# Kernel tuning notes

Measured on AMD Instinct MI355X. Metric: run time of the kernel, lower is better.

The kernel has to match this reference:

```python
import jax, jax.numpy as jnp
import numpy as np

EMBED_DIM = 128
NUM_HEADS = 4
HEAD_DIM = EMBED_DIM // NUM_HEADS


def setup_inputs() -> dict:
    key = jax.random.key(0)
    ks = jax.random.split(key, 9)
    B, C, H, W = 8, EMBED_DIM, 64, 64
    s = 1.0 / np.sqrt(EMBED_DIM)
    x = jax.random.normal(ks[0], (B, C, H, W), dtype=jnp.float32)
    Wq = jax.random.uniform(ks[1], (EMBED_DIM, EMBED_DIM), jnp.float32, -s, s)
    bq = jax.random.uniform(ks[2], (EMBED_DIM,), jnp.float32, -s, s)
    Wk = jax.random.uniform(ks[3], (EMBED_DIM, EMBED_DIM), jnp.float32, -s, s)
    bk = jax.random.uniform(ks[4], (EMBED_DIM,), jnp.float32, -s, s)
    Wv = jax.random.uniform(ks[5], (EMBED_DIM, EMBED_DIM), jnp.float32, -s, s)
    bv = jax.random.uniform(ks[6], (EMBED_DIM,), jnp.float32, -s, s)
    Wo = jax.random.uniform(ks[7], (EMBED_DIM, EMBED_DIM), jnp.float32, -s, s)
    bo = jax.random.uniform(ks[8], (EMBED_DIM,), jnp.float32, -s, s)
    return {"x": x, "Wq": Wq, "bq": bq, "Wk": Wk, "bk": bk,
            "Wv": Wv, "bv": bv, "Wo": Wo, "bo": bo}


def reference(x, Wq, bq, Wk, bk, Wv, bv, Wo, bo):
    B, C, H, W = x.shape
    N = H * W
    # (B, C, H, W) -> (B, N, C) tokens
    t = x.reshape(B, C, N).transpose(0, 2, 1)
    # torch Linear: y = t @ W.T + b
    Q = t @ Wq.T + bq
    K = t @ Wk.T + bk
    V = t @ Wv.T + bv
    # split heads: (B, heads, N, head_dim)
    Q = Q.reshape(B, N, NUM_HEADS, HEAD_DIM).transpose(0, 2, 1, 3)
    K = K.reshape(B, N, NUM_HEADS, HEAD_DIM).transpose(0, 2, 1, 3)
    V = V.reshape(B, N, NUM_HEADS, HEAD_DIM).transpose(0, 2, 1, 3)
    scale = 1.0 / np.sqrt(HEAD_DIM).astype(np.float32)
    attn = jnp.einsum('bhnd,bhmd->bhnm', Q, K) * scale  # (B,h,N,N)
    attn = jax.nn.softmax(attn, axis=-1)
    out = jnp.einsum('bhnm,bhmd->bhnd', attn, V)
    out = out.transpose(0, 2, 1, 3).reshape(B, N, EMBED_DIM)
    out = out @ Wo.T + bo
    return out.transpose(0, 2, 1).reshape(B, EMBED_DIM, H, W)
```

## Files before the change

kernel.cpp:

```cpp
#include <hip/hip_runtime.h>


using f32x4  = __attribute__((ext_vector_type(4))) float;
using bf16x8 = __attribute__((ext_vector_type(8))) short;

#define QSCALE 0.17677669529663687f
#define LOG2E  1.4426950408889634f
#define QKS    (QSCALE * LOG2E)

static __device__ __forceinline__ unsigned short f2bf(float f) {
    union { float f; unsigned int u; } v; v.f = f;
    unsigned int r = v.u + 0x7FFFu + ((v.u >> 16) & 1u);
    return (unsigned short)(r >> 16);
}

static __device__ __forceinline__ f32x4 mfma16(bf16x8 a, bf16x8 b, f32x4 c) {
    return __builtin_amdgcn_mfma_f32_16x16x32_bf16(a, b, c, 0, 0, 0);
}

__global__ __launch_bounds__(256) void k_prep(
    const float* __restrict__ x,
    const float* __restrict__ Wq, const float* __restrict__ Wk,
    const float* __restrict__ Wv, const float* __restrict__ Wo,
    unsigned short* __restrict__ t_bf, unsigned short* __restrict__ Wb)
{
    const int bx = blockIdx.x;
    const int tid = threadIdx.x;
    if (bx >= 1024) {
        const int m = bx - 1024;
        const float* W = (m == 0) ? Wq : (m == 1) ? Wk : (m == 2) ? Wv : Wo;
        const float s = (m == 0) ? QKS : 1.0f;
        for (int idx = tid; idx < 16384; idx += 256)
            Wb[m * 16384 + idx] = f2bf(W[idx] * s);
        return;
    }
    __shared__ float tl[64][65];
    const int b  = bx >> 7;
    const int c0 = ((bx >> 6) & 1) * 64;
    const int n0 = (bx & 63) * 64;
    for (int idx = tid; idx < 4096; idx += 256) {
        const int ci = idx >> 6, nj = idx & 63;
        tl[ci][nj] = x[((size_t)(b * 128 + c0 + ci)) * 4096 + n0 + nj];
    }
    __syncthreads();
    for (int idx = tid; idx < 4096; idx += 256) {
        const int nj = idx >> 6, ci = idx & 63;
        t_bf[((size_t)(b * 4096 + n0 + nj)) * 128 + c0 + ci] = f2bf(tl[ci][nj]);
    }
}

__global__ __launch_bounds__(256) void k_proj3(
    const unsigned short* __restrict__ t_bf, const unsigned short* __restrict__ Wb,
    const float* __restrict__ bq, const float* __restrict__ bk, const float* __restrict__ bv,
    unsigned short* __restrict__ Qb, unsigned short* __restrict__ Kb,
    unsigned short* __restrict__ Vt)
{
    const int mat  = blockIdx.y;
    const int widx = threadIdx.x >> 6;
    const int lane = threadIdx.x & 63;
    const int g = lane >> 4, l15 = lane & 15;
    const int row0 = blockIdx.x * 64 + widx * 16;
    const int gt_row = row0 + l15;
    const unsigned short* Wm = Wb + mat * 16384;
    const float* bias = (mat == 0) ? bq : (mat == 1) ? bk : bv;

    bf16x8 tf[4];
    #pragma unroll
    for (int kc = 0; kc < 4; ++kc)
        tf[kc] = *(const bf16x8*)(t_bf + (size_t)gt_row * 128 + kc * 32 + g * 8);

    #pragma unroll
    for (int ot = 0; ot < 8; ++ot) {
        f32x4 acc;
        if (mat < 2) {
            float bb = bias[ot * 16 + l15];
            if (mat == 0) bb *= QKS;
            acc[0] = bb; acc[1] = bb; acc[2] = bb; acc[3] = bb;
        } else {
            #pragma unroll
            for (int r = 0; r < 4; ++r) acc[r] = bias[ot * 16 + 4 * g + r];
        }
        #pragma unroll
        for (int kc = 0; kc < 4; ++kc) {
            bf16x8 wf = *(const bf16x8*)(Wm + (size_t)(ot * 16 + l15) * 128 + kc * 32 + g * 8);
            acc = (mat == 2) ? mfma16(wf, tf[kc], acc) : mfma16(tf[kc], wf, acc);
        }
        if (mat < 2) {
            unsigned short* dst = (mat == 0) ? Qb : Kb;
            const int o = ot * 16 + l15, h = o >> 5, d = o & 31;
            #pragma unroll
            for (int r = 0; r < 4; ++r) {
                const int gt = row0 + 4 * g + r;
                const int b = gt >> 12, n = gt & 4095;
                dst[(((size_t)(b * 4 + h)) * 4096 + n) * 32 + d] = f2bf(acc[r]);
            }
        } else {
            const int b = gt_row >> 12, n = gt_row & 4095;
            const int n31 = n & 31;
            const int pos = ((n31 >> 2) & 3) * 8 + ((n31 >> 4) & 1) * 4 + (n31 & 3);
            #pragma unroll
            for (int r = 0; r < 4; ++r) {
                const int o = ot * 16 + 4 * g + r, h2 = o >> 5, d = o & 31;
                const size_t tb2 = ((size_t)(b * 4 + h2) * 128 + ((n >> 5) & 127)) * 1024;
                Vt[tb2 + d * 32 + pos] = f2bf(acc[r]);
            }
        }
    }
}

__global__ __launch_bounds__(256) void k_attn(
    const unsigned short* __restrict__ Qb, const unsigned short* __restrict__ Kb,
    const unsigned short* __restrict__ Vt, unsigned short* __restrict__ Ob)
{
    const int bid = blockIdx.x;
    const int swz = (bid & 7) * 512 + (bid >> 3);
    const int widx = threadIdx.x >> 6;
    const int bh = swz >> 7, q0 = (swz & 127) * 32;
    const int lane = threadIdx.x & 63, g = lane >> 4, l15 = lane & 15;

    __shared__ float lacc[3][32][36];
    __shared__ float lden[3][32];

    const bf16x8 qf0 = *(const bf16x8*)(Qb + ((size_t)bh * 4096 + q0 + l15) * 32 + g * 8);
    const bf16x8 qf1 = *(const bf16x8*)(Qb + ((size_t)bh * 4096 + q0 + 16 + l15) * 32 + g * 8);

    const unsigned short* kp = Kb + (size_t)bh * 131072
                             + (size_t)(widx * 1024 + l15) * 32 + g * 8;
    const unsigned short* vp = Vt + (size_t)bh * 131072 + (size_t)widx * 32768
                             + l15 * 32 + g * 8;

    bf16x8 onesf;
    #pragma unroll
    for (int j = 0; j < 8; ++j) onesf[j] = (short)0x3F80;

    f32x4 acc00 = {0.f,0.f,0.f,0.f}, acc01 = {0.f,0.f,0.f,0.f};
    f32x4 acc10 = {0.f,0.f,0.f,0.f}, acc11 = {0.f,0.f,0.f,0.f};
    f32x4 acc20 = {0.f,0.f,0.f,0.f}, acc21 = {0.f,0.f,0.f,0.f};
    const f32x4 z = {0.f,0.f,0.f,0.f};

    #pragma unroll 2
    for (int it = 0; it < 32; ++it) {
        const bf16x8 kf0 = *(const bf16x8*)(kp);
        const bf16x8 kf1 = *(const bf16x8*)(kp + 512);
        const bf16x8 vf0 = *(const bf16x8*)(vp);
        const bf16x8 vf1 = *(const bf16x8*)(vp + 512);
        kp += 1024;
        vp += 1024;

        f32x4 s00 = mfma16(kf0, qf0, z), s01 = mfma16(kf1, qf0, z);
        f32x4 s10 = mfma16(kf0, qf1, z), s11 = mfma16(kf1, qf1, z);

        bf16x8 pa0, pa1;
        #pragma unroll
        for (int i = 0; i < 4; ++i) {
            pa0[i]     = (short)f2bf(__builtin_amdgcn_exp2f(s00[i]));
            pa0[4 + i] = (short)f2bf(__builtin_amdgcn_exp2f(s01[i]));
            pa1[i]     = (short)f2bf(__builtin_amdgcn_exp2f(s10[i]));
            pa1[4 + i] = (short)f2bf(__builtin_amdgcn_exp2f(s11[i]));
        }

        acc00 = mfma16(pa0, vf0, acc00);
        acc01 = mfma16(pa0, vf1, acc01);
        acc20 = mfma16(pa0, onesf, acc20);
        acc10 = mfma16(pa1, vf0, acc10);
        acc11 = mfma16(pa1, vf1, acc11);
        acc21 = mfma16(pa1, onesf, acc21);
    }

    if (widx != 0) {
        const int s = widx - 1;
        *(f32x4*)&lacc[s][l15][4 * g]           = acc00;
        *(f32x4*)&lacc[s][16 + l15][4 * g]      = acc01;
        *(f32x4*)&lacc[s][l15][16 + 4 * g]      = acc10;
        *(f32x4*)&lacc[s][16 + l15][16 + 4 * g] = acc11;
        if (l15 == 0) {
            #pragma unroll
            for (int r = 0; r < 4; ++r) {
                lden[s][4 * g + r]      = acc20[r];
                lden[s][16 + 4 * g + r] = acc21[r];
            }
        }
    }
    __syncthreads();
    if (widx != 0) return;

    const int b = bh >> 2, h = bh & 3;
    #pragma unroll
    for (int r = 0; r < 4; ++r) {
        const int row0 = 4 * g + r, row1 = 16 + 4 * g + r;
        const float rd0 = 1.0f / (acc20[r] + lden[0][row0] + lden[1][row0] + lden[2][row0]);
        const float rd1 = 1.0f / (acc21[r] + lden[0][row1] + lden[1][row1] + lden[2][row1]);
        const float o00 = acc00[r] + lacc[0][l15][row0]      + lacc[1][l15][row0]      + lacc[2][l15][row0];
        const float o01 = acc01[r] + lacc[0][16 + l15][row0] + lacc[1][16 + l15][row0] + lacc[2][16 + l15][row0];
        const float o10 = acc10[r] + lacc[0][l15][row1]      + lacc[1][l15][row1]      + lacc[2][l15][row1];
        const float o11 = acc11[r] + lacc[0][16 + l15][row1] + lacc[1][16 + l15][row1] + lacc[2][16 + l15][row1];
        const size_t base0 = ((size_t)b * 4096 + q0 + row0) * 128 + h * 32;
        const size_t base1 = ((size_t)b * 4096 + q0 + row1) * 128 + h * 32;
        Ob[base0 + l15]      = f2bf(o00 * rd0);
        Ob[base0 + 16 + l15] = f2bf(o01 * rd0);
        Ob[base1 + l15]      = f2bf(o10 * rd1);
        Ob[base1 + 16 + l15] = f2bf(o11 * rd1);
    }
}

__global__ __launch_bounds__(256) void k_projo(
    const unsigned short* __restrict__ Ob, const unsigned short* __restrict__ Wob,
    const float* __restrict__ bo, float* __restrict__ out)
{
    const int widx = threadIdx.x >> 6;
    const int lane = threadIdx.x & 63, g = lane >> 4, l15 = lane & 15;
    const int gt = blockIdx.x * 64 + widx * 16 + l15;
    const int b = gt >> 12, n = gt & 4095;

    bf16x8 of[4];
    #pragma unroll
    for (int kc = 0; kc < 4; ++kc)
        of[kc] = *(const bf16x8*)(Ob + (size_t)gt * 128 + kc * 32 + g * 8);

    #pragma unroll
    for (int ot = 0; ot < 8; ++ot) {
        f32x4 acc;
        #pragma unroll
        for (int r = 0; r < 4; ++r) acc[r] = bo[ot * 16 + 4 * g + r];
        #pragma unroll
        for (int kc = 0; kc < 4; ++kc) {
            bf16x8 wf = *(const bf16x8*)(Wob + (size_t)(ot * 16 + l15) * 128 + kc * 32 + g * 8);
            acc = mfma16(wf, of[kc], acc);
        }
        #pragma unroll
        for (int r = 0; r < 4; ++r)
            out[((size_t)b * 128 + ot * 16 + 4 * g + r) * 4096 + n] = acc[r];
    }
}

extern "C" void kernel_launch(void* const* d_in, const int* in_sizes, int n_in,
                              void* d_out, int out_size, void* d_ws, size_t ws_size,
                              hipStream_t stream)
{
    const float* x  = (const float*)d_in[0];
    const float* Wq = (const float*)d_in[1];
    const float* bq = (const float*)d_in[2];
    const float* Wk = (const float*)d_in[3];
    const float* bk = (const float*)d_in[4];
    const float* Wv = (const float*)d_in[5];
    const float* bv = (const float*)d_in[6];
    const float* Wo = (const float*)d_in[7];
    const float* bo = (const float*)d_in[8];
    float* out = (float*)d_out;

    char* ws = (char*)d_ws;
    unsigned short* t_bf = (unsigned short*)(ws);
    unsigned short* Wb   = (unsigned short*)(ws +  8388608);
    unsigned short* Qb   = (unsigned short*)(ws +  8519680);
    unsigned short* Kb   = (unsigned short*)(ws + 16908288);
    unsigned short* Vt   = (unsigned short*)(ws + 25296896);
    unsigned short* Ob   = (unsigned short*)(ws + 33685504);

    k_prep <<<dim3(1028),     dim3(256), 0, stream>>>(x, Wq, Wk, Wv, Wo, t_bf, Wb);
    k_proj3<<<dim3(512, 3),   dim3(256), 0, stream>>>(t_bf, Wb, bq, bk, bv, Qb, Kb, Vt);
    k_attn <<<dim3(4096),     dim3(256), 0, stream>>>(Qb, Kb, Vt, Ob);
    k_projo<<<dim3(512),      dim3(256), 0, stream>>>(Ob, Wb + 3 * 16384, bo, out);
}
```

Before: 184.7 us.

## Process 64 queries per attention block to reuse K/V loads across four fragments

The attention kernel now handles 64 query rows per block instead of 32, so each K/V fragment loaded from global memory feeds four query fragments rather than two, and the grid is halved. It also replaces the manual round-to-nearest bf16 conversion of the exponentiated scores with native __bf16 casts, which may lower to hardware conversion instructions. The trade-off is more accumulator registers and shared memory per block, which may reduce occupancy, and fewer blocks across the GPU.

```diff
diff --git a/kernel.cpp b/kernel.cpp
--- a/kernel.cpp
+++ b/kernel.cpp
@@ -3,6 +3,7 @@
 
 using f32x4  = __attribute__((ext_vector_type(4))) float;
 using bf16x8 = __attribute__((ext_vector_type(8))) short;
+using bfv8   = __attribute__((ext_vector_type(8))) __bf16;
 
 #define QSCALE 0.17677669529663687f
 #define LOG2E  1.4426950408889634f
@@ -113,16 +114,18 @@
     const unsigned short* __restrict__ Vt, unsigned short* __restrict__ Ob)
 {
     const int bid = blockIdx.x;
-    const int swz = (bid & 7) * 512 + (bid >> 3);
+    const int swz = (bid & 7) * 256 + (bid >> 3);
     const int widx = threadIdx.x >> 6;
-    const int bh = swz >> 7, q0 = (swz & 127) * 32;
+    const int bh = swz >> 6, q0 = (swz & 63) * 64;
     const int lane = threadIdx.x & 63, g = lane >> 4, l15 = lane & 15;
 
-    __shared__ float lacc[3][32][36];
-    __shared__ float lden[3][32];
-
-    const bf16x8 qf0 = *(const bf16x8*)(Qb + ((size_t)bh * 4096 + q0 + l15) * 32 + g * 8);
-    const bf16x8 qf1 = *(const bf16x8*)(Qb + ((size_t)bh * 4096 + q0 + 16 + l15) * 32 + g * 8);
+    __shared__ float lacc[3][32][68];
+    __shared__ float lden[3][64];
+
+    bf16x8 qf[4];
+    #pragma unroll
+    for (int f = 0; f < 4; ++f)
+        qf[f] = *(const bf16x8*)(Qb + ((size_t)bh * 4096 + q0 + f * 16 + l15) * 32 + g * 8);
 
     const unsigned short* kp = Kb + (size_t)bh * 131072
                              + (size_t)(widx * 1024 + l15) * 32 + g * 8;
@@ -133,12 +136,16 @@
     #pragma unroll
     for (int j = 0; j < 8; ++j) onesf[j] = (short)0x3F80;
 
-    f32x4 acc00 = {0.f,0.f,0.f,0.f}, acc01 = {0.f,0.f,0.f,0.f};
-    f32x4 acc10 = {0.f,0.f,0.f,0.f}, acc11 = {0.f,0.f,0.f,0.f};
-    f32x4 acc20 = {0.f,0.f,0.f,0.f}, acc21 = {0.f,0.f,0.f,0.f};
+    f32x4 aO[4][2];
+    f32x4 aD[4];
+    #pragma unroll
+    for (int f = 0; f < 4; ++f) {
+        aO[f][0] = f32x4{0.f,0.f,0.f,0.f};
+        aO[f][1] = f32x4{0.f,0.f,0.f,0.f};
+        aD[f]    = f32x4{0.f,0.f,0.f,0.f};
+    }
     const f32x4 z = {0.f,0.f,0.f,0.f};
 
-    #pragma unroll 2
     for (int it = 0; it < 32; ++it) {
         const bf16x8 kf0 = *(const bf16x8*)(kp);
         const bf16x8 kf1 = *(const bf16x8*)(kp + 512);
@@ -147,37 +154,33 @@
         kp += 1024;
         vp += 1024;
 
-        f32x4 s00 = mfma16(kf0, qf0, z), s01 = mfma16(kf1, qf0, z);
-        f32x4 s10 = mfma16(kf0, qf1, z), s11 = mfma16(kf1, qf1, z);
-
-        bf16x8 pa0, pa1;
-        #pragma unroll
-        for (int i = 0; i < 4; ++i) {
-            pa0[i]     = (short)f2bf(__builtin_amdgcn_exp2f(s00[i]));
-            pa0[4 + i] = (short)f2bf(__builtin_amdgcn_exp2f(s01[i]));
-            pa1[i]     = (short)f2bf(__builtin_amdgcn_exp2f(s10[i]));
-            pa1[4 + i] = (short)f2bf(__builtin_amdgcn_exp2f(s11[i]));
-        }
-
-        acc00 = mfma16(pa0, vf0, acc00);
-        acc01 = mfma16(pa0, vf1, acc01);
-        acc20 = mfma16(pa0, onesf, acc20);
-        acc10 = mfma16(pa1, vf0, acc10);
-        acc11 = mfma16(pa1, vf1, acc11);
-        acc21 = mfma16(pa1, onesf, acc21);
+        #pragma unroll
+        for (int f = 0; f < 4; ++f) {
+            const f32x4 s0 = mfma16(kf0, qf[f], z);
+            const f32x4 s1 = mfma16(kf1, qf[f], z);
+            bfv8 pb;
+            #pragma unroll
+            for (int i = 0; i < 4; ++i) {
+                pb[i]     = (__bf16)__builtin_amdgcn_exp2f(s0[i]);
+                pb[4 + i] = (__bf16)__builtin_amdgcn_exp2f(s1[i]);
+            }
+            const bf16x8 pa = __builtin_bit_cast(bf16x8, pb);
+            aO[f][0] = mfma16(pa, vf0, aO[f][0]);
+            aO[f][1] = mfma16(pa, vf1, aO[f][1]);
+            aD[f]    = mfma16(pa, onesf, aD[f]);
+        }
     }
 
     if (widx != 0) {
         const int s = widx - 1;
-        *(f32x4*)&lacc[s][l15][4 * g]           = acc00;
-        *(f32x4*)&lacc[s][16 + l15][4 * g]      = acc01;
-        *(f32x4*)&lacc[s][l15][16 + 4 * g]      = acc10;
-        *(f32x4*)&lacc[s][16 + l15][16 + 4 * g] = acc11;
-        if (l15 == 0) {
-            #pragma unroll
-            for (int r = 0; r < 4; ++r) {
-                lden[s][4 * g + r]      = acc20[r];
-                lden[s][16 + 4 * g + r] = acc21[r];
+        #pragma unroll
+        for (int f = 0; f < 4; ++f) {
+            *(f32x4*)&lacc[s][l15][f * 16 + 4 * g]      = aO[f][0];
+            *(f32x4*)&lacc[s][16 + l15][f * 16 + 4 * g] = aO[f][1];
+            if (l15 == 0) {
+                #pragma unroll
+                for (int r = 0; r < 4; ++r)
+                    lden[s][f * 16 + 4 * g + r] = aD[f][r];
             }
         }
     }
@@ -186,20 +189,19 @@
 
     const int b = bh >> 2, h = bh & 3;
     #pragma unroll
-    for (int r = 0; r < 4; ++r) {
-        const int row0 = 4 * g + r, row1 = 16 + 4 * g + r;
-        const float rd0 = 1.0f / (acc20[r] + lden[0][row0] + lden[1][row0] + lden[2][row0]);
-        const float rd1 = 1.0f / (acc21[r] + lden[0][row1] + lden[1][row1] + lden[2][row1]);
-        const float o00 = acc00[r] + lacc[0][l15][row0]      + lacc[1][l15][row0]      + lacc[2][l15][row0];
-        const float o01 = acc01[r] + lacc[0][16 + l15][row0] + lacc[1][16 + l15][row0] + lacc[2][16 + l15][row0];
-        const float o10 = acc10[r] + lacc[0][l15][row1]      + lacc[1][l15][row1]      + lacc[2][l15][row1];
-        const float o11 = acc11[r] + lacc[0][16 + l15][row1] + lacc[1][16 + l15][row1] + lacc[2][16 + l15][row1];
-        const size_t base0 = ((size_t)b * 4096 + q0 + row0) * 128 + h * 32;
-        const size_t base1 = ((size_t)b * 4096 + q0 + row1) * 128 + h * 32;
-        Ob[base0 + l15]      = f2bf(o00 * rd0);
-        Ob[base0 + 16 + l15] = f2bf(o01 * rd0);
-        Ob[base1 + l15]      = f2bf(o10 * rd1);
-        Ob[base1 + 16 + l15] = f2bf(o11 * rd1);
+    for (int f = 0; f < 4; ++f) {
+        #pragma unroll
+        for (int r = 0; r < 4; ++r) {
+            const int row = f * 16 + 4 * g + r;
+            const float rd = 1.0f / (aD[f][r] + lden[0][row] + lden[1][row] + lden[2][row]);
+            const float o0 = aO[f][0][r] + lacc[0][l15][row]
+                           + lacc[1][l15][row] + lacc[2][l15][row];
+            const float o1 = aO[f][1][r] + lacc[0][16 + l15][row]
+                           + lacc[1][16 + l15][row] + lacc[2][16 + l15][row];
+            const size_t base = ((size_t)b * 4096 + q0 + row) * 128 + h * 32;
+            Ob[base + l15]      = f2bf(o0 * rd);
+            Ob[base + 16 + l15] = f2bf(o1 * rd);
+        }
     }
 }
 
@@ -258,6 +260,6 @@
 
     k_prep <<<dim3(1028),     dim3(256), 0, stream>>>(x, Wq, Wk, Wv, Wo, t_bf, Wb);
     k_proj3<<<dim3(512, 3),   dim3(256), 0, stream>>>(t_bf, Wb, bq, bk, bv, Qb, Kb, Vt);
-    k_attn <<<dim3(4096),     dim3(256), 0, stream>>>(Qb, Kb, Vt, Ob);
+    k_attn <<<dim3(2048),     dim3(256), 0, stream>>>(Qb, Kb, Vt, Ob);
     k_projo<<<dim3(512),      dim3(256), 0, stream>>>(Ob, Wb + 3 * 16384, bo, out);
 }
```

Result: faster. 173.9 us (-5.9%).
